# Optimization experiments

Measured on AMD Instinct MI355X. Metric: run time of the kernel, lower is better.

## Reference

```python
import jax, jax.numpy as jnp
import numpy as np

L, N1, N2 = 2, 2, 2
E1 = sum(1 + i for i in range(N1))      # 3 first-stage DAG edges per layer
E2 = sum(N1 + i for i in range(N2))     # 5 last-stage DAG edges per layer
DIM, IN_DIM, NUM_CLASSES = 256, 128, 10
N_NODES, N_EDGES, N_GRAPHS = 8000, 128000, 64


def setup_inputs():
    key = jax.random.key(0)
    ks = jax.random.split(key, 16)
    s = 0.05  # weight scale to keep activations bounded through stacked cells
    return {
        'h': jax.random.normal(ks[0], (N_NODES, IN_DIM), jnp.float32),
        'W_emb': jax.random.normal(ks[1], (IN_DIM, DIM), jnp.float32) * s,
        'b_emb': jnp.zeros((DIM,), jnp.float32),
        'Wf_dense': jax.random.normal(ks[2], (L, E1, DIM, DIM), jnp.float32) * s,
        'bf_dense': jnp.zeros((L, E1, DIM), jnp.float32),
        'Wf_sparse': jax.random.normal(ks[3], (L, E1, DIM, DIM), jnp.float32) * s,
        'bf_sparse': jnp.zeros((L, E1, DIM), jnp.float32),
        'Wl_dense': jax.random.normal(ks[4], (L, E2, DIM, DIM), jnp.float32) * s,
        'bl_dense': jnp.zeros((L, E2, DIM), jnp.float32),
        'Wl_sparse': jax.random.normal(ks[5], (L, E2, DIM, DIM), jnp.float32) * s,
        'bl_sparse': jnp.zeros((L, E2, DIM), jnp.float32),
        'a_first': 0.001 * jax.random.normal(ks[6], (L * E1, 4), jnp.float32),
        'a_mid': 0.001 * jax.random.normal(ks[7], (L * N1, 4), jnp.float32),
        'a_last': 0.001 * jax.random.normal(ks[8], (L * E2, 4), jnp.float32),
        'C1': jax.random.normal(ks[9], (DIM, DIM // 2), jnp.float32) * s,
        'c1b': jnp.zeros((DIM // 2,), jnp.float32),
        'C2': jax.random.normal(ks[10], (DIM // 2, DIM // 4), jnp.float32) * s,
        'c2b': jnp.zeros((DIM // 4,), jnp.float32),
        'C3': jax.random.normal(ks[11], (DIM // 4, NUM_CLASSES), jnp.float32) * s,
        'c3b': jnp.zeros((NUM_CLASSES,), jnp.float32),
        'src': jax.random.randint(ks[12], (N_EDGES,), 0, N_NODES, jnp.int32),
        'dst': jax.random.randint(ks[13], (N_EDGES,), 0, N_NODES, jnp.int32),
        'graph_ids': jnp.sort(jax.random.randint(ks[14], (N_NODES,), 0, N_GRAPHS, jnp.int32)),
        'num_graphs': N_GRAPHS,
    }


def forward(h, W_emb, b_emb, Wf_dense, bf_dense, Wf_sparse, bf_sparse,
            Wl_dense, bl_dense, Wl_sparse, bl_sparse, a_first, a_mid, a_last,
            C1, c1b, C2, c2b, C3, c3b, src, dst, graph_ids, num_graphs):
    N = h.shape[0]
    deg0 = jax.ops.segment_sum(jnp.ones((src.shape[0],), h.dtype), dst, num_segments=N)
    deg = jnp.maximum(deg0, 1.0)[:, None]      # in-degree, clamped for mean
    has_nb = (deg0 > 0)[:, None]

    # DARTS softmax over candidate ops (per DAG edge)
    wf = jax.nn.softmax(a_first, axis=1)
    wm = jax.nn.softmax(a_mid, axis=1)
    wl = jax.nn.softmax(a_last, axis=1)

    def mixed(xj, w, Wd, bd, Ws, bs):
        # mixture over {f_zero, f_identity, f_dense, f_sparse}
        dense = xj @ Wd + bd
        agg = jax.ops.segment_sum(xj[src], dst, num_segments=N) / deg  # mean msg-passing
        sparse = agg @ Ws + bs
        return w[1] * xj + w[2] * dense + w[3] * sparse  # w[0]*zero omitted

    x = h @ W_emb + b_emb  # embedding (Linear, data_type='gc')
    for l in range(L):
        # first stage: DAG over N1 intermediate nodes
        states = [x]
        e = 0
        for n in range(1, N1 + 1):
            s = jnp.zeros_like(x)
            for j in range(n):
                s = s + mixed(states[j], wf[l * E1 + e], Wf_dense[l, e], bf_dense[l, e],
                              Wf_sparse[l, e], bf_sparse[l, e])
                e += 1
            states.append(jax.nn.relu(s))
        # middle stage: mixture over {identity, max, mean, sum} neighbor aggregators
        mids = []
        for n in range(N1):
            xn = states[n + 1]
            w = wm[l * N1 + n]
            msg = xn[src]
            msum = jax.ops.segment_sum(msg, dst, num_segments=N)
            mmean = msum / deg
            mmax = jnp.where(has_nb, jax.ops.segment_max(msg, dst, num_segments=N), 0.0)
            mids.append(w[0] * xn + w[1] * mmax + w[2] * mmean + w[3] * msum)
        # last stage: DAG over N2 output nodes, inputs = middle states + prior lasts
        lasts = []
        e = 0
        for n in range(N2):
            ins = mids + lasts
            s = jnp.zeros_like(x)
            for j in range(N1 + n):
                s = s + mixed(ins[j], wl[l * E2 + e], Wl_dense[l, e], bl_dense[l, e],
                              Wl_sparse[l, e], bl_sparse[l, e])
                e += 1
            lasts.append(jax.nn.relu(s))
        x = x + sum(lasts) / float(N2)  # residual cell output

    # dgl.mean_nodes readout: per-graph mean over nodes
    cnt = jnp.maximum(jax.ops.segment_sum(jnp.ones((N,), x.dtype), graph_ids,
                                          num_segments=num_graphs), 1.0)[:, None]
    hg = jax.ops.segment_sum(x, graph_ids, num_segments=num_graphs) / cnt
    # MLPReadout: 256 -> 128 -> 64 -> 10
    y = jax.nn.relu(hg @ C1 + c1b)
    y = jax.nn.relu(y @ C2 + c2b)
    return y @ C3 + c3b


def reference(h, W_emb, b_emb, Wf_dense, bf_dense, Wf_sparse, bf_sparse,
              Wl_dense, bl_dense, Wl_sparse, bl_sparse, a_first, a_mid, a_last,
              C1, c1b, C2, c2b, C3, c3b, src, dst, graph_ids, num_graphs):
    return forward(h, W_emb, b_emb, Wf_dense, bf_dense, Wf_sparse, bf_sparse,
                   Wl_dense, bl_dense, Wl_sparse, bl_sparse, a_first, a_mid, a_last,
                   C1, c1b, C2, c2b, C3, c3b, src, dst, graph_ids, num_graphs)
```

## Files before the change

kernel.cpp:

```cpp
#include <hip/hip_runtime.h>

#define N_NODES   8000
#define M_PAD     8192
#define PADR      (M_PAD - N_NODES)
#define N_EDGES   128000
#define N_GRAPHS  64
#define DIM       256
#define IN_DIM    128

typedef short bf16x8 __attribute__((ext_vector_type(8)));
typedef float f32x4 __attribute__((ext_vector_type(4)));

static __device__ __forceinline__ float bf2f(unsigned v) {
  return __uint_as_float(v << 16);
}
static __device__ __forceinline__ unsigned f2bf(float f) {
  unsigned u = __float_as_uint(f);
  return (u + 0x7fffu + ((u >> 16) & 1u)) >> 16;
}

__global__ __launch_bounds__(256) void k_init(int* __restrict__ counts,
                                              unsigned short* __restrict__ hpad,
                                              unsigned short* __restrict__ p0,
                                              unsigned short* __restrict__ p1,
                                              unsigned short* __restrict__ p2,
                                              unsigned short* __restrict__ p3) {
  int i = blockIdx.x * 256 + threadIdx.x;
  if (i < N_NODES) counts[i] = 0;
  if (i < PADR * IN_DIM) hpad[i] = 0;
  if (i < PADR * DIM) { p0[i] = 0; p1[i] = 0; p2[i] = 0; p3[i] = 0; }
}

__global__ __launch_bounds__(256) void k_count(const int* __restrict__ dst,
                                               int* __restrict__ counts) {
  int e = blockIdx.x * 256 + threadIdx.x;
  if (e < N_EDGES) atomicAdd(&counts[dst[e]], 1);
}

__global__ __launch_bounds__(256) void k_scan(const int* __restrict__ counts,
                                              int* __restrict__ row_ofs,
                                              int* __restrict__ cursor,
                                              float* __restrict__ invdeg) {
  __shared__ int chunk[256];
  const int per = (N_NODES + 255) / 256;
  int t = threadIdx.x;
  int base = t * per;
  int s = 0;
  for (int i = 0; i < per; ++i) {
    int idx = base + i;
    if (idx < N_NODES) s += counts[idx];
  }
  chunk[t] = s;
  __syncthreads();
  for (int off = 1; off < 256; off <<= 1) {
    int v = 0;
    if (t >= off) v = chunk[t - off];
    __syncthreads();
    if (t >= off) chunk[t] += v;
    __syncthreads();
  }
  int run = (t > 0) ? chunk[t - 1] : 0;
  for (int i = 0; i < per; ++i) {
    int idx = base + i;
    if (idx < N_NODES) {
      row_ofs[idx] = run;
      cursor[idx] = run;
      int c = counts[idx];
      invdeg[idx] = 1.0f / (float)(c > 1 ? c : 1);
      run += c;
    }
  }
  if (t == 0) row_ofs[N_NODES] = chunk[255];
}

__global__ __launch_bounds__(256) void k_fill(const int* __restrict__ src,
                                              const int* __restrict__ dst,
                                              int* __restrict__ cursor,
                                              int* __restrict__ csr_src) {
  int e = blockIdx.x * 256 + threadIdx.x;
  if (e < N_EDGES) {
    int p = atomicAdd(&cursor[dst[e]], 1);
    csr_src[p] = src[e];
  }
}

__global__ __launch_bounds__(64) void k_softmax(const float* __restrict__ af,
                                                const float* __restrict__ am,
                                                const float* __restrict__ al,
                                                float* __restrict__ w) {
  int t = threadIdx.x;
  const float* sp;
  float* dp;
  if (t < 6)       { sp = af + t * 4;        dp = w + t * 4; }
  else if (t < 10) { sp = am + (t - 6) * 4;  dp = w + 24 + (t - 6) * 4; }
  else if (t < 20) { sp = al + (t - 10) * 4; dp = w + 40 + (t - 10) * 4; }
  else return;
  float a0 = sp[0], a1 = sp[1], a2 = sp[2], a3 = sp[3];
  float m = fmaxf(fmaxf(a0, a1), fmaxf(a2, a3));
  float e0 = expf(a0 - m), e1 = expf(a1 - m), e2 = expf(a2 - m), e3 = expf(a3 - m);
  float si = 1.0f / (e0 + e1 + e2 + e3);
  dp[0] = e0 * si; dp[1] = e1 * si; dp[2] = e2 * si; dp[3] = e3 * si;
}

__global__ __launch_bounds__(256) void k_cvt_bf16(const float* __restrict__ in,
                                                  unsigned short* __restrict__ out,
                                                  int n) {
  int i = blockIdx.x * 256 + threadIdx.x;
  if (i < n) out[i] = (unsigned short)f2bf(in[i]);
}

__global__ __launch_bounds__(256) void k_transpose_cvt(const float* __restrict__ in,
                                                       unsigned short* __restrict__ out,
                                                       int K, int N) {
  __shared__ float tile[32][33];
  int k0 = blockIdx.x * 32, n0 = blockIdx.y * 32;
  int tx = threadIdx.x & 31, ty = threadIdx.x >> 5;
#pragma unroll
  for (int i = 0; i < 4; ++i)
    tile[ty + 8 * i][tx] = in[(size_t)(k0 + ty + 8 * i) * N + n0 + tx];
  __syncthreads();
#pragma unroll
  for (int i = 0; i < 4; ++i)
    out[(size_t)(n0 + ty + 8 * i) * K + k0 + tx] =
        (unsigned short)f2bf(tile[tx][ty + 8 * i]);
}

__global__ __launch_bounds__(256) void k_transpose_cvt32(const float* __restrict__ Wfd,
                                                         const float* __restrict__ Wfs,
                                                         const float* __restrict__ Wld,
                                                         const float* __restrict__ Wls,
                                                         const float* __restrict__ wsoft,
                                                         unsigned short* __restrict__ out) {
  __shared__ float tile[32][33];
  int z = blockIdx.z;
  const float* in;
  float coef;
  const float* wf = wsoft;
  const float* wl = wsoft + 40;
  if (z < 6)       { in = Wfd + (size_t)z * DIM * DIM;        coef = wf[z * 4 + 2]; }
  else if (z < 12) { in = Wfs + (size_t)(z - 6) * DIM * DIM;  coef = wf[(z - 6) * 4 + 3]; }
  else if (z < 22) { in = Wld + (size_t)(z - 12) * DIM * DIM; coef = wl[(z - 12) * 4 + 2]; }
  else             { in = Wls + (size_t)(z - 22) * DIM * DIM; coef = wl[(z - 22) * 4 + 3]; }
  unsigned short* o = out + (size_t)z * DIM * DIM;
  int k0 = blockIdx.x * 32, n0 = blockIdx.y * 32;
  int tx = threadIdx.x & 31, ty = threadIdx.x >> 5;
#pragma unroll
  for (int i = 0; i < 4; ++i)
    tile[ty + 8 * i][tx] = in[(size_t)(k0 + ty + 8 * i) * DIM + n0 + tx];
  __syncthreads();
#pragma unroll
  for (int i = 0; i < 4; ++i)
    o[(size_t)(n0 + ty + 8 * i) * DIM + k0 + tx] =
        (unsigned short)f2bf(coef * tile[tx][ty + 8 * i]);
}

#define SEG_ACC(u) \
  { s0 += bf2f((u).x & 0xffffu); s1 += bf2f((u).x >> 16); \
    s2 += bf2f((u).y & 0xffffu); s3 += bf2f((u).y >> 16); }

#define MID_ACC(u) \
  { float v0 = bf2f((u).x & 0xffffu), v1 = bf2f((u).x >> 16); \
    float v2 = bf2f((u).y & 0xffffu), v3 = bf2f((u).y >> 16); \
    s0 += v0; s1 += v1; s2 += v2; s3 += v3; \
    m0 = fmaxf(m0, v0); m1 = fmaxf(m1, v1); \
    m2 = fmaxf(m2, v2); m3 = fmaxf(m3, v3); }

__global__ __launch_bounds__(256) void k_segmean_bf(const unsigned short* __restrict__ X,
                                                    const int* __restrict__ row_ofs,
                                                    const int* __restrict__ csr_src,
                                                    const float* __restrict__ invdeg,
                                                    unsigned short* __restrict__ out) {
  int node = blockIdx.x * 4 + (threadIdx.x >> 6);
  int l = threadIdx.x & 63;
  if (node >= N_NODES) return;
  int beg = row_ofs[node], end = row_ofs[node + 1];
  float s0 = 0.f, s1 = 0.f, s2 = 0.f, s3 = 0.f;
  int e = beg;
  for (; e + 8 <= end; e += 8) {
    int i0 = csr_src[e], i1 = csr_src[e + 1], i2 = csr_src[e + 2], i3 = csr_src[e + 3];
    int i4 = csr_src[e + 4], i5 = csr_src[e + 5], i6 = csr_src[e + 6], i7 = csr_src[e + 7];
    uint2 u0 = *(const uint2*)&X[(size_t)i0 * DIM + 4 * l];
    uint2 u1 = *(const uint2*)&X[(size_t)i1 * DIM + 4 * l];
    uint2 u2 = *(const uint2*)&X[(size_t)i2 * DIM + 4 * l];
    uint2 u3 = *(const uint2*)&X[(size_t)i3 * DIM + 4 * l];
    uint2 u4 = *(const uint2*)&X[(size_t)i4 * DIM + 4 * l];
    uint2 u5 = *(const uint2*)&X[(size_t)i5 * DIM + 4 * l];
    uint2 u6 = *(const uint2*)&X[(size_t)i6 * DIM + 4 * l];
    uint2 u7 = *(const uint2*)&X[(size_t)i7 * DIM + 4 * l];
    SEG_ACC(u0) SEG_ACC(u1) SEG_ACC(u2) SEG_ACC(u3)
    SEG_ACC(u4) SEG_ACC(u5) SEG_ACC(u6) SEG_ACC(u7)
  }
  for (; e + 4 <= end; e += 4) {
    int i0 = csr_src[e], i1 = csr_src[e + 1], i2 = csr_src[e + 2], i3 = csr_src[e + 3];
    uint2 u0 = *(const uint2*)&X[(size_t)i0 * DIM + 4 * l];
    uint2 u1 = *(const uint2*)&X[(size_t)i1 * DIM + 4 * l];
    uint2 u2 = *(const uint2*)&X[(size_t)i2 * DIM + 4 * l];
    uint2 u3 = *(const uint2*)&X[(size_t)i3 * DIM + 4 * l];
    SEG_ACC(u0) SEG_ACC(u1) SEG_ACC(u2) SEG_ACC(u3)
  }
  for (; e < end; ++e) {
    uint2 u = *(const uint2*)&X[(size_t)csr_src[e] * DIM + 4 * l];
    SEG_ACC(u)
  }
  float iv = invdeg[node];
  uint2 o;
  o.x = f2bf(s0 * iv) | (f2bf(s1 * iv) << 16);
  o.y = f2bf(s2 * iv) | (f2bf(s3 * iv) << 16);
  *(uint2*)&out[(size_t)node * DIM + 4 * l] = o;
}

__global__ __launch_bounds__(256) void k_segmean2_bf(const unsigned short* __restrict__ X0,
                                                     const unsigned short* __restrict__ X1,
                                                     const int* __restrict__ row_ofs,
                                                     const int* __restrict__ csr_src,
                                                     const float* __restrict__ invdeg,
                                                     unsigned short* __restrict__ out0,
                                                     unsigned short* __restrict__ out1) {
  int node = blockIdx.x * 4 + (threadIdx.x >> 6);
  int l = threadIdx.x & 63;
  if (node >= N_NODES) return;
  int beg = row_ofs[node], end = row_ofs[node + 1];
  float a0 = 0.f, a1 = 0.f, a2 = 0.f, a3 = 0.f;
  float b0 = 0.f, b1 = 0.f, b2 = 0.f, b3 = 0.f;
  int e = beg;
  for (; e + 4 <= end; e += 4) {
    size_t r0 = (size_t)csr_src[e] * DIM + 4 * l;
    size_t r1 = (size_t)csr_src[e + 1] * DIM + 4 * l;
    size_t r2 = (size_t)csr_src[e + 2] * DIM + 4 * l;
    size_t r3 = (size_t)csr_src[e + 3] * DIM + 4 * l;
    uint2 u0 = *(const uint2*)&X0[r0];
    uint2 u1 = *(const uint2*)&X0[r1];
    uint2 u2 = *(const uint2*)&X0[r2];
    uint2 u3 = *(const uint2*)&X0[r3];
    uint2 v0 = *(const uint2*)&X1[r0];
    uint2 v1 = *(const uint2*)&X1[r1];
    uint2 v2 = *(const uint2*)&X1[r2];
    uint2 v3 = *(const uint2*)&X1[r3];
    a0 += bf2f(u0.x & 0xffffu) + bf2f(u1.x & 0xffffu) + bf2f(u2.x & 0xffffu) + bf2f(u3.x & 0xffffu);
    a1 += bf2f(u0.x >> 16) + bf2f(u1.x >> 16) + bf2f(u2.x >> 16) + bf2f(u3.x >> 16);
    a2 += bf2f(u0.y & 0xffffu) + bf2f(u1.y & 0xffffu) + bf2f(u2.y & 0xffffu) + bf2f(u3.y & 0xffffu);
    a3 += bf2f(u0.y >> 16) + bf2f(u1.y >> 16) + bf2f(u2.y >> 16) + bf2f(u3.y >> 16);
    b0 += bf2f(v0.x & 0xffffu) + bf2f(v1.x & 0xffffu) + bf2f(v2.x & 0xffffu) + bf2f(v3.x & 0xffffu);
    b1 += bf2f(v0.x >> 16) + bf2f(v1.x >> 16) + bf2f(v2.x >> 16) + bf2f(v3.x >> 16);
    b2 += bf2f(v0.y & 0xffffu) + bf2f(v1.y & 0xffffu) + bf2f(v2.y & 0xffffu) + bf2f(v3.y & 0xffffu);
    b3 += bf2f(v0.y >> 16) + bf2f(v1.y >> 16) + bf2f(v2.y >> 16) + bf2f(v3.y >> 16);
  }
  for (; e < end; ++e) {
    size_t rb = (size_t)csr_src[e] * DIM + 4 * l;
    uint2 u = *(const uint2*)&X0[rb];
    uint2 v = *(const uint2*)&X1[rb];
    a0 += bf2f(u.x & 0xffffu); a1 += bf2f(u.x >> 16);
    a2 += bf2f(u.y & 0xffffu); a3 += bf2f(u.y >> 16);
    b0 += bf2f(v.x & 0xffffu); b1 += bf2f(v.x >> 16);
    b2 += bf2f(v.y & 0xffffu); b3 += bf2f(v.y >> 16);
  }
  float iv = invdeg[node];
  uint2 o;
  o.x = f2bf(a0 * iv) | (f2bf(a1 * iv) << 16);
  o.y = f2bf(a2 * iv) | (f2bf(a3 * iv) << 16);
  *(uint2*)&out0[(size_t)node * DIM + 4 * l] = o;
  o.x = f2bf(b0 * iv) | (f2bf(b1 * iv) << 16);
  o.y = f2bf(b2 * iv) | (f2bf(b3 * iv) << 16);
  *(uint2*)&out1[(size_t)node * DIM + 4 * l] = o;
}

__global__ __launch_bounds__(256) void k_segmid_bf(const unsigned short* __restrict__ Xn,
                                                   const int* __restrict__ row_ofs,
                                                   const int* __restrict__ csr_src,
                                                   const float* __restrict__ invdeg,
                                                   const float* __restrict__ wrow,
                                                   unsigned short* __restrict__ mean_out,
                                                   unsigned short* __restrict__ mids_out) {
  int node = blockIdx.x * 4 + (threadIdx.x >> 6);
  int l = threadIdx.x & 63;
  if (node >= N_NODES) return;
  int beg = row_ofs[node], end = row_ofs[node + 1];
  float s0 = 0.f, s1 = 0.f, s2 = 0.f, s3 = 0.f;
  float m0 = 0.f, m1 = 0.f, m2 = 0.f, m3 = 0.f;
  int e = beg;
  for (; e + 8 <= end; e += 8) {
    int i0 = csr_src[e], i1 = csr_src[e + 1], i2 = csr_src[e + 2], i3 = csr_src[e + 3];
    int i4 = csr_src[e + 4], i5 = csr_src[e + 5], i6 = csr_src[e + 6], i7 = csr_src[e + 7];
    uint2 u0 = *(const uint2*)&Xn[(size_t)i0 * DIM + 4 * l];
    uint2 u1 = *(const uint2*)&Xn[(size_t)i1 * DIM + 4 * l];
    uint2 u2 = *(const uint2*)&Xn[(size_t)i2 * DIM + 4 * l];
    uint2 u3 = *(const uint2*)&Xn[(size_t)i3 * DIM + 4 * l];
    uint2 u4 = *(const uint2*)&Xn[(size_t)i4 * DIM + 4 * l];
    uint2 u5 = *(const uint2*)&Xn[(size_t)i5 * DIM + 4 * l];
    uint2 u6 = *(const uint2*)&Xn[(size_t)i6 * DIM + 4 * l];
    uint2 u7 = *(const uint2*)&Xn[(size_t)i7 * DIM + 4 * l];
    MID_ACC(u0) MID_ACC(u1) MID_ACC(u2) MID_ACC(u3)
    MID_ACC(u4) MID_ACC(u5) MID_ACC(u6) MID_ACC(u7)
  }
  for (; e + 4 <= end; e += 4) {
    int i0 = csr_src[e], i1 = csr_src[e + 1], i2 = csr_src[e + 2], i3 = csr_src[e + 3];
    uint2 u0 = *(const uint2*)&Xn[(size_t)i0 * DIM + 4 * l];
    uint2 u1 = *(const uint2*)&Xn[(size_t)i1 * DIM + 4 * l];
    uint2 u2 = *(const uint2*)&Xn[(size_t)i2 * DIM + 4 * l];
    uint2 u3 = *(const uint2*)&Xn[(size_t)i3 * DIM + 4 * l];
    MID_ACC(u0) MID_ACC(u1) MID_ACC(u2) MID_ACC(u3)
  }
  for (; e < end; ++e) {
    uint2 u = *(const uint2*)&Xn[(size_t)csr_src[e] * DIM + 4 * l];
    MID_ACC(u)
  }
  float iv = invdeg[node];
  float e0 = s0 * iv, e1 = s1 * iv, e2 = s2 * iv, e3 = s3 * iv;
  if (mean_out) {
    uint2 o;
    o.x = f2bf(e0) | (f2bf(e1) << 16);
    o.y = f2bf(e2) | (f2bf(e3) << 16);
    *(uint2*)&mean_out[(size_t)node * DIM + 4 * l] = o;
  }
  float w0 = wrow[0], w1 = wrow[1], w2 = wrow[2], w3 = wrow[3];
  uint2 xu = *(const uint2*)&Xn[(size_t)node * DIM + 4 * l];
  float x0 = bf2f(xu.x & 0xffffu), x1 = bf2f(xu.x >> 16);
  float x2 = bf2f(xu.y & 0xffffu), x3 = bf2f(xu.y >> 16);
  uint2 o;
  o.x = f2bf(w0 * x0 + w1 * m0 + w2 * e0 + w3 * s0) |
        (f2bf(w0 * x1 + w1 * m1 + w2 * e1 + w3 * s1) << 16);
  o.y = f2bf(w0 * x2 + w1 * m2 + w2 * e2 + w3 * s2) |
        (f2bf(w0 * x3 + w1 * m3 + w2 * e3 + w3 * s3) << 16);
  *(uint2*)&mids_out[(size_t)node * DIM + 4 * l] = o;
}

struct GemmDescW {
  const unsigned short* A[4];
  const unsigned short* W[2][4];
  const float* b[2][4];
  const float* c[2][4];
  const unsigned short* I[2];
  const float* ic[2][2];
  const float* pre[2];
  const float* resid[2];
  const unsigned short* addl[2];
  float* out_f32[2];
  unsigned short* out_bf[2];
  int nmat, nid, K, relu[2], colshift;
};

__global__ __launch_bounds__(256) void k_gemm_mfma(GemmDescW d) {
  __shared__ __align__(16) unsigned short As[2][64][72];
  __shared__ __align__(16) unsigned short Bs[2][64][72];
  const int tid = threadIdx.x;
  const int b = blockIdx.x;
  const int cs = d.colshift;
  const int c = (b >> 3) & ((1 << cs) - 1);
  const int bm = ((b & 7) + 8 * (b >> (3 + cs))) * 64;
  const int half = c >> 2;
  const int bn = (c & 3) * 64;
  const int w = tid >> 6, l = tid & 63;
  const int wm = (w >> 1) * 32, wn = (w & 1) * 32;
  const int lr = l & 15, lk = (l >> 4) * 8;
  const int ldr = tid >> 3, ldk = (tid & 7) * 8;

  const int K = d.K;
  const int kds = (K == 256) ? 2 : 1;
  const int kmask = (1 << kds) - 1;
  const int nsteps = d.nmat << kds;

  f32x4 zero = {0.f, 0.f, 0.f, 0.f};
  f32x4 acc[2][2];
  acc[0][0] = zero; acc[0][1] = zero; acc[1][0] = zero; acc[1][1] = zero;

  auto gload = [&](int s, uint4& a0, uint4& a1, uint4& b0, uint4& b1) {
    int t = s >> kds;
    int k0 = (s & kmask) << 6;
    const unsigned short* __restrict__ A = d.A[t];
    const unsigned short* __restrict__ W = d.W[half][t];
    a0 = *(const uint4*)&A[(size_t)(bm + ldr) * K + k0 + ldk];
    a1 = *(const uint4*)&A[(size_t)(bm + ldr + 32) * K + k0 + ldk];
    b0 = *(const uint4*)&W[(size_t)(bn + ldr) * K + k0 + ldk];
    b1 = *(const uint4*)&W[(size_t)(bn + ldr + 32) * K + k0 + ldk];
  };

  {
    uint4 a0, a1, b0, b1;
    gload(0, a0, a1, b0, b1);
    *(uint4*)&As[0][ldr][ldk] = a0;
    *(uint4*)&As[0][ldr + 32][ldk] = a1;
    *(uint4*)&Bs[0][ldr][ldk] = b0;
    *(uint4*)&Bs[0][ldr + 32][ldk] = b1;
  }
  __syncthreads();

  int buf = 0;
  for (int s = 0; s < nsteps; ++s) {
    uint4 na0, na1, nb0, nb1;
    const bool more = (s + 1 < nsteps);
    if (more) gload(s + 1, na0, na1, nb0, nb1);
#pragma unroll
    for (int ks = 0; ks < 2; ++ks) {
      bf16x8 a0 = *(const bf16x8*)&As[buf][wm + lr][ks * 32 + lk];
      bf16x8 a1 = *(const bf16x8*)&As[buf][wm + 16 + lr][ks * 32 + lk];
      bf16x8 b0 = *(const bf16x8*)&Bs[buf][wn + lr][ks * 32 + lk];
      bf16x8 b1 = *(const bf16x8*)&Bs[buf][wn + 16 + lr][ks * 32 + lk];
      acc[0][0] = __builtin_amdgcn_mfma_f32_16x16x32_bf16(a0, b0, acc[0][0], 0, 0, 0);
      acc[0][1] = __builtin_amdgcn_mfma_f32_16x16x32_bf16(a0, b1, acc[0][1], 0, 0, 0);
      acc[1][0] = __builtin_amdgcn_mfma_f32_16x16x32_bf16(a1, b0, acc[1][0], 0, 0, 0);
      acc[1][1] = __builtin_amdgcn_mfma_f32_16x16x32_bf16(a1, b1, acc[1][1], 0, 0, 0);
    }
    if (more) {
      *(uint4*)&As[buf ^ 1][ldr][ldk] = na0;
      *(uint4*)&As[buf ^ 1][ldr + 32][ldk] = na1;
      *(uint4*)&Bs[buf ^ 1][ldr][ldk] = nb0;
      *(uint4*)&Bs[buf ^ 1][ldr + 32][ldk] = nb1;
    }
    __syncthreads();
    buf ^= 1;
  }

  float bias[2] = {0.f, 0.f};
  for (int t = 0; t < d.nmat; ++t) {
    const float* bp = d.b[half][t];
    if (bp) {
      float cc = d.c[half][t] ? *d.c[half][t] : 1.0f;
      bias[0] += cc * bp[bn + wn + lr];
      bias[1] += cc * bp[bn + wn + 16 + lr];
    }
  }
  float vout[2][2][4];
#pragma unroll
  for (int m = 0; m < 2; ++m)
#pragma unroll
    for (int n = 0; n < 2; ++n)
#pragma unroll
      for (int i = 0; i < 4; ++i) vout[m][n][i] = acc[m][n][i] + bias[n];
#pragma unroll
  for (int u = 0; u < 2; ++u) {
    if (u < d.nid) {
      float icu = *d.ic[half][u];
      const unsigned short* __restrict__ I = d.I[u];
#pragma unroll
      for (int m = 0; m < 2; ++m)
#pragma unroll
        for (int n = 0; n < 2; ++n)
#pragma unroll
          for (int i = 0; i < 4; ++i) {
            int row = bm + wm + m * 16 + (l >> 4) * 4 + i;
            int col = bn + wn + n * 16 + lr;
            vout[m][n][i] += icu * bf2f(I[(size_t)row * DIM + col]);
          }
    }
  }
  const float* pre = d.pre[half];
  const float* resid = d.resid[half];
  const unsigned short* addl = d.addl[half];
  unsigned short* obf = d.out_bf[half];
  float* of32 = d.out_f32[half];
  const int do_relu = d.relu[half];
#pragma unroll
  for (int m = 0; m < 2; ++m)
#pragma unroll
    for (int n = 0; n < 2; ++n)
#pragma unroll
      for (int i = 0; i < 4; ++i) {
        int row = bm + wm + m * 16 + (l >> 4) * 4 + i;
        int col = bn + wn + n * 16 + lr;
        size_t idx = (size_t)row * DIM + col;
        float v = vout[m][n][i];
        if (pre) v += pre[idx];
        if (do_relu) v = fmaxf(v, 0.f);
        if (resid) v = resid[idx] + 0.5f * (bf2f(addl[idx]) + v);
        if (obf) obf[idx] = (unsigned short)f2bf(v);
        if (of32) of32[idx] = v;
      }
}

__global__ __launch_bounds__(256) void k_readout_mlp(const float* __restrict__ x,
                                                     const int* __restrict__ gid,
                                                     const float* __restrict__ C1,
                                                     const float* __restrict__ c1b,
                                                     const float* __restrict__ C2,
                                                     const float* __restrict__ c2b,
                                                     const float* __restrict__ C3,
                                                     const float* __restrict__ c3b,
                                                     float* __restrict__ out) {
  int g = blockIdx.x, t = threadIdx.x;
  int lo = 0, hi = N_NODES;
  while (lo < hi) { int m = (lo + hi) >> 1; if (gid[m] < g) lo = m + 1; else hi = m; }
  int beg = lo;
  lo = beg; hi = N_NODES;
  while (lo < hi) { int m = (lo + hi) >> 1; if (gid[m] <= g) lo = m + 1; else hi = m; }
  int end = lo;
  float s0 = 0.f, s1 = 0.f, s2 = 0.f, s3 = 0.f;
  float s4 = 0.f, s5 = 0.f, s6 = 0.f, s7 = 0.f;
  int i = beg;
  for (; i + 8 <= end; i += 8) {
    s0 += x[(size_t)(i + 0) * DIM + t];
    s1 += x[(size_t)(i + 1) * DIM + t];
    s2 += x[(size_t)(i + 2) * DIM + t];
    s3 += x[(size_t)(i + 3) * DIM + t];
    s4 += x[(size_t)(i + 4) * DIM + t];
    s5 += x[(size_t)(i + 5) * DIM + t];
    s6 += x[(size_t)(i + 6) * DIM + t];
    s7 += x[(size_t)(i + 7) * DIM + t];
  }
  for (; i < end; ++i) s0 += x[(size_t)i * DIM + t];
  float s = ((s0 + s1) + (s2 + s3)) + ((s4 + s5) + (s6 + s7));
  int cnt = end - beg;
  __shared__ float h0[256], h1[128], h2[64];
  h0[t] = s / (float)(cnt > 1 ? cnt : 1);
  __syncthreads();
  if (t < 128) {
    float v = c1b[t];
    for (int k = 0; k < 256; ++k) v = fmaf(h0[k], C1[k * 128 + t], v);
    h1[t] = fmaxf(v, 0.f);
  }
  __syncthreads();
  if (t < 64) {
    float v = c2b[t];
    for (int k = 0; k < 128; ++k) v = fmaf(h1[k], C2[k * 64 + t], v);
    h2[t] = fmaxf(v, 0.f);
  }
  __syncthreads();
  if (t < 10) {
    float v = c3b[t];
    for (int k = 0; k < 64; ++k) v = fmaf(h2[k], C3[k * 10 + t], v);
    out[g * 10 + t] = v;
  }
}

extern "C" void kernel_launch(void* const* d_in, const int* in_sizes, int n_in,
                              void* d_out, int out_size, void* d_ws, size_t ws_size,
                              hipStream_t stream) {
  const float* h     = (const float*)d_in[0];
  const float* W_emb = (const float*)d_in[1];
  const float* b_emb = (const float*)d_in[2];
  const float* Wf_d  = (const float*)d_in[3];
  const float* bf_d  = (const float*)d_in[4];
  const float* Wf_s  = (const float*)d_in[5];
  const float* bf_s  = (const float*)d_in[6];
  const float* Wl_d  = (const float*)d_in[7];
  const float* bl_d  = (const float*)d_in[8];
  const float* Wl_s  = (const float*)d_in[9];
  const float* bl_s  = (const float*)d_in[10];
  const float* a_first = (const float*)d_in[11];
  const float* a_mid   = (const float*)d_in[12];
  const float* a_last  = (const float*)d_in[13];
  const float* C1 = (const float*)d_in[14];
  const float* c1b = (const float*)d_in[15];
  const float* C2 = (const float*)d_in[16];
  const float* c2b = (const float*)d_in[17];
  const float* C3 = (const float*)d_in[18];
  const float* c3b = (const float*)d_in[19];
  const int* src = (const int*)d_in[20];
  const int* dst = (const int*)d_in[21];
  const int* gid = (const int*)d_in[22];
  (void)in_sizes; (void)n_in; (void)out_size; (void)ws_size;

  char* p = (char*)d_ws;
  auto alloc = [&](size_t bytes) {
    void* r = (void*)p;
    p += (bytes + 255) & ~(size_t)255;
    return r;
  };
  typedef unsigned short u16;
  const size_t NBF = (size_t)M_PAD * DIM * sizeof(u16);
  float* x_f32  = (float*)alloc((size_t)M_PAD * DIM * sizeof(float));
  float* s2part = (float*)alloc((size_t)M_PAD * DIM * sizeof(float));
  float* xpart  = (float*)alloc((size_t)M_PAD * DIM * sizeof(float));
  u16* xb    = (u16*)alloc(NBF);
  u16* s1b   = (u16*)alloc(NBF);
  u16* s2b   = (u16*)alloc(NBF);
  u16* m0b   = (u16*)alloc(NBF);
  u16* m1b   = (u16*)alloc(NBF);
  u16* l0b   = (u16*)alloc(NBF);
  u16* aggAb = (u16*)alloc(NBF);
  u16* aggBb = (u16*)alloc(NBF);
  u16* h_bf  = (u16*)alloc((size_t)M_PAD * IN_DIM * sizeof(u16));
  u16* WT    = (u16*)alloc((size_t)(DIM * IN_DIM + 32 * DIM * DIM) * sizeof(u16));
  u16* WTe   = WT;
  u16* WTfd  = WT + DIM * IN_DIM;
  u16* WTfs  = WTfd + 6 * DIM * DIM;
  u16* WTld  = WTfs + 6 * DIM * DIM;
  u16* WTls  = WTld + 10 * DIM * DIM;
  float* invdeg = (float*)alloc(N_NODES * sizeof(float));
  int* counts  = (int*)alloc(N_NODES * sizeof(int));
  int* row_ofs = (int*)alloc((N_NODES + 1) * sizeof(int));
  int* cursor  = (int*)alloc(N_NODES * sizeof(int));
  int* csr_src = (int*)alloc(N_EDGES * sizeof(int));
  float* wsoft = (float*)alloc(80 * sizeof(float));

  const int EB = (N_EDGES + 255) / 256;

  k_init<<<192, 256, 0, stream>>>(
      counts, h_bf + (size_t)N_NODES * IN_DIM,
      aggAb + (size_t)N_NODES * DIM, aggBb + (size_t)N_NODES * DIM,
      m0b + (size_t)N_NODES * DIM, m1b + (size_t)N_NODES * DIM);

  k_count<<<EB, 256, 0, stream>>>(dst, counts);
  k_scan<<<1, 256, 0, stream>>>(counts, row_ofs, cursor, invdeg);
  k_fill<<<EB, 256, 0, stream>>>(src, dst, cursor, csr_src);
  k_softmax<<<1, 64, 0, stream>>>(a_first, a_mid, a_last, wsoft);

  const float* wf = wsoft;
  const float* wm = wsoft + 24;
  const float* wl = wsoft + 40;

  k_cvt_bf16<<<(N_NODES * IN_DIM + 255) / 256, 256, 0, stream>>>(h, h_bf, N_NODES * IN_DIM);
  k_transpose_cvt<<<dim3(IN_DIM / 32, DIM / 32, 1), 256, 0, stream>>>(W_emb, WTe, IN_DIM, DIM);
  k_transpose_cvt32<<<dim3(8, 8, 32), 256, 0, stream>>>(Wf_d, Wf_s, Wl_d, Wl_s, wsoft, WTfd);

  const int GG1 = (M_PAD / 64) * 4;
  const int GG2 = (M_PAD / 64) * 8;
  const int SB = (N_NODES + 3) / 4;

  {
    GemmDescW d{};
    d.A[0] = h_bf; d.W[0][0] = WTe; d.b[0][0] = b_emb;
    d.nmat = 1; d.nid = 0; d.K = IN_DIM; d.colshift = 2;
    d.out_f32[0] = x_f32; d.out_bf[0] = xb;
    k_gemm_mfma<<<GG1, 256, 0, stream>>>(d);
  }

  for (int l = 0; l < 2; ++l) {
    auto WFD = [&](int e) { return WTfd + (size_t)(l * 3 + e) * DIM * DIM; };
    auto BFD = [&](int e) { return bf_d + (size_t)(l * 3 + e) * DIM; };
    auto WFS = [&](int e) { return WTfs + (size_t)(l * 3 + e) * DIM * DIM; };
    auto BFS = [&](int e) { return bf_s + (size_t)(l * 3 + e) * DIM; };
    auto WLD = [&](int e) { return WTld + (size_t)(l * 5 + e) * DIM * DIM; };
    auto BLD = [&](int e) { return bl_d + (size_t)(l * 5 + e) * DIM; };
    auto WLS = [&](int e) { return WTls + (size_t)(l * 5 + e) * DIM * DIM; };
    auto BLS = [&](int e) { return bl_s + (size_t)(l * 5 + e) * DIM; };
    auto WFrow = [&](int e) { return wf + (l * 3 + e) * 4; };
    auto WMrow = [&](int n) { return wm + (l * 2 + n) * 4; };
    auto WLrow = [&](int e) { return wl + (l * 5 + e) * 4; };

    k_segmean_bf<<<SB, 256, 0, stream>>>(xb, row_ofs, csr_src, invdeg, aggAb);

    {
      GemmDescW d{};
      d.A[0] = xb; d.A[1] = aggAb; d.nmat = 2; d.K = DIM; d.colshift = 3;
      d.I[0] = xb; d.nid = 1;
      d.W[0][0] = WFD(0); d.b[0][0] = BFD(0); d.c[0][0] = WFrow(0) + 2;
      d.W[0][1] = WFS(0); d.b[0][1] = BFS(0); d.c[0][1] = WFrow(0) + 3;
      d.ic[0][0] = WFrow(0) + 1; d.relu[0] = 1; d.out_bf[0] = s1b;
      d.W[1][0] = WFD(1); d.b[1][0] = BFD(1); d.c[1][0] = WFrow(1) + 2;
      d.W[1][1] = WFS(1); d.b[1][1] = BFS(1); d.c[1][1] = WFrow(1) + 3;
      d.ic[1][0] = WFrow(1) + 1; d.relu[1] = 0; d.out_f32[1] = s2part;
      k_gemm_mfma<<<GG2, 256, 0, stream>>>(d);
    }

    k_segmid_bf<<<SB, 256, 0, stream>>>(s1b, row_ofs, csr_src, invdeg, WMrow(0), aggBb, m0b);

    {
      GemmDescW d{};
      d.A[0] = s1b; d.A[1] = aggBb; d.nmat = 2; d.K = DIM; d.colshift = 2;
      d.I[0] = s1b; d.nid = 1;
      d.W[0][0] = WFD(2); d.b[0][0] = BFD(2); d.c[0][0] = WFrow(2) + 2;
      d.W[0][1] = WFS(2); d.b[0][1] = BFS(2); d.c[0][1] = WFrow(2) + 3;
      d.ic[0][0] = WFrow(2) + 1; d.pre[0] = s2part; d.relu[0] = 1; d.out_bf[0] = s2b;
      k_gemm_mfma<<<GG1, 256, 0, stream>>>(d);
    }

    k_segmid_bf<<<SB, 256, 0, stream>>>(s2b, row_ofs, csr_src, invdeg, WMrow(1), nullptr, m1b);

    k_segmean2_bf<<<SB, 256, 0, stream>>>(m0b, m1b, row_ofs, csr_src, invdeg, aggAb, aggBb);

    {
      GemmDescW d{};
      d.A[0] = m0b; d.A[1] = aggAb; d.A[2] = m1b; d.A[3] = aggBb;
      d.nmat = 4; d.K = DIM; d.colshift = 3;
      d.I[0] = m0b; d.I[1] = m1b; d.nid = 2;
      d.W[0][0] = WLD(0); d.b[0][0] = BLD(0); d.c[0][0] = WLrow(0) + 2;
      d.W[0][1] = WLS(0); d.b[0][1] = BLS(0); d.c[0][1] = WLrow(0) + 3;
      d.W[0][2] = WLD(1); d.b[0][2] = BLD(1); d.c[0][2] = WLrow(1) + 2;
      d.W[0][3] = WLS(1); d.b[0][3] = BLS(1); d.c[0][3] = WLrow(1) + 3;
      d.ic[0][0] = WLrow(0) + 1; d.ic[0][1] = WLrow(1) + 1;
      d.relu[0] = 1; d.out_bf[0] = l0b;
      d.W[1][0] = WLD(2); d.b[1][0] = BLD(2); d.c[1][0] = WLrow(2) + 2;
      d.W[1][1] = WLS(2); d.b[1][1] = BLS(2); d.c[1][1] = WLrow(2) + 3;
      d.W[1][2] = WLD(3); d.b[1][2] = BLD(3); d.c[1][2] = WLrow(3) + 2;
      d.W[1][3] = WLS(3); d.b[1][3] = BLS(3); d.c[1][3] = WLrow(3) + 3;
      d.ic[1][0] = WLrow(2) + 1; d.ic[1][1] = WLrow(3) + 1;
      d.relu[1] = 0; d.out_f32[1] = xpart;
      k_gemm_mfma<<<GG2, 256, 0, stream>>>(d);
    }

    k_segmean_bf<<<SB, 256, 0, stream>>>(l0b, row_ofs, csr_src, invdeg, s1b);

    {
      GemmDescW d{};
      d.A[0] = l0b; d.A[1] = s1b; d.nmat = 2; d.K = DIM; d.colshift = 2;
      d.I[0] = l0b; d.nid = 1;
      d.W[0][0] = WLD(4); d.b[0][0] = BLD(4); d.c[0][0] = WLrow(4) + 2;
      d.W[0][1] = WLS(4); d.b[0][1] = BLS(4); d.c[0][1] = WLrow(4) + 3;
      d.ic[0][0] = WLrow(4) + 1; d.pre[0] = xpart; d.relu[0] = 1;
      d.resid[0] = x_f32; d.addl[0] = l0b;
      d.out_f32[0] = x_f32; d.out_bf[0] = xb;
      k_gemm_mfma<<<GG1, 256, 0, stream>>>(d);
    }
  }

  k_readout_mlp<<<N_GRAPHS, 256, 0, stream>>>(x_f32, gid, C1, c1b, C2, c2b, C3, c3b,
                                              (float*)d_out);
}
```

Measured before the change: 326.9 us.

## Prefetch two k-steps ahead in MFMA GEMM and merge embedding weight transpose launch

The GEMM main loop is restructured into a two-step unrolled pipeline that keeps two register stages of global loads in flight, so global memory latency is hidden further ahead of the MFMA work. nsteps is always even (nmat<<kds with kds>=1), so the paired loop covers every step. The separate W_emb transpose kernel is folded into the batched weight transpose kernel as an extra z-slice, removing one launch. The deeper prefetch raises register pressure, which could lower occupancy.

```diff
diff --git a/kernel.cpp b/kernel.cpp
--- a/kernel.cpp
+++ b/kernel.cpp
@@ -109,30 +109,30 @@
   if (i < n) out[i] = (unsigned short)f2bf(in[i]);
 }
 
-__global__ __launch_bounds__(256) void k_transpose_cvt(const float* __restrict__ in,
-                                                       unsigned short* __restrict__ out,
-                                                       int K, int N) {
-  __shared__ float tile[32][33];
-  int k0 = blockIdx.x * 32, n0 = blockIdx.y * 32;
-  int tx = threadIdx.x & 31, ty = threadIdx.x >> 5;
-#pragma unroll
-  for (int i = 0; i < 4; ++i)
-    tile[ty + 8 * i][tx] = in[(size_t)(k0 + ty + 8 * i) * N + n0 + tx];
-  __syncthreads();
-#pragma unroll
-  for (int i = 0; i < 4; ++i)
-    out[(size_t)(n0 + ty + 8 * i) * K + k0 + tx] =
-        (unsigned short)f2bf(tile[tx][ty + 8 * i]);
-}
-
-__global__ __launch_bounds__(256) void k_transpose_cvt32(const float* __restrict__ Wfd,
+__global__ __launch_bounds__(256) void k_transpose_cvt33(const float* __restrict__ Wfd,
                                                          const float* __restrict__ Wfs,
                                                          const float* __restrict__ Wld,
                                                          const float* __restrict__ Wls,
                                                          const float* __restrict__ wsoft,
-                                                         unsigned short* __restrict__ out) {
+                                                         unsigned short* __restrict__ out,
+                                                         const float* __restrict__ W_emb,
+                                                         unsigned short* __restrict__ WTe) {
   __shared__ float tile[32][33];
   int z = blockIdx.z;
+  int tx = threadIdx.x & 31, ty = threadIdx.x >> 5;
+  if (z == 32) {
+    if (blockIdx.x >= 4) return;
+    int k0 = blockIdx.x * 32, n0 = blockIdx.y * 32;
+#pragma unroll
+    for (int i = 0; i < 4; ++i)
+      tile[ty + 8 * i][tx] = W_emb[(size_t)(k0 + ty + 8 * i) * DIM + n0 + tx];
+    __syncthreads();
+#pragma unroll
+    for (int i = 0; i < 4; ++i)
+      WTe[(size_t)(n0 + ty + 8 * i) * IN_DIM + k0 + tx] =
+          (unsigned short)f2bf(tile[tx][ty + 8 * i]);
+    return;
+  }
   const float* in;
   float coef;
   const float* wf = wsoft;
@@ -143,7 +143,6 @@
   else             { in = Wls + (size_t)(z - 22) * DIM * DIM; coef = wl[(z - 22) * 4 + 3]; }
   unsigned short* o = out + (size_t)z * DIM * DIM;
   int k0 = blockIdx.x * 32, n0 = blockIdx.y * 32;
-  int tx = threadIdx.x & 31, ty = threadIdx.x >> 5;
 #pragma unroll
   for (int i = 0; i < 4; ++i)
     tile[ty + 8 * i][tx] = in[(size_t)(k0 + ty + 8 * i) * DIM + n0 + tx];
@@ -373,42 +372,47 @@
     b0 = *(const uint4*)&W[(size_t)(bn + ldr) * K + k0 + ldk];
     b1 = *(const uint4*)&W[(size_t)(bn + ldr + 32) * K + k0 + ldk];
   };
-
-  {
-    uint4 a0, a1, b0, b1;
-    gload(0, a0, a1, b0, b1);
-    *(uint4*)&As[0][ldr][ldk] = a0;
-    *(uint4*)&As[0][ldr + 32][ldk] = a1;
-    *(uint4*)&Bs[0][ldr][ldk] = b0;
-    *(uint4*)&Bs[0][ldr + 32][ldk] = b1;
-  }
+  auto lstore = [&](int buf, uint4 a0, uint4 a1, uint4 b0, uint4 b1) {
+    *(uint4*)&As[buf][ldr][ldk] = a0;
+    *(uint4*)&As[buf][ldr + 32][ldk] = a1;
+    *(uint4*)&Bs[buf][ldr][ldk] = b0;
+    *(uint4*)&Bs[buf][ldr + 32][ldk] = b1;
+  };
+
+  uint4 ra0, ra1, ra2, ra3;
+  uint4 rb0, rb1, rb2, rb3;
+
+  gload(0, ra0, ra1, ra2, ra3);
+  gload(1, rb0, rb1, rb2, rb3);
+  lstore(0, ra0, ra1, ra2, ra3);
   __syncthreads();
 
-  int buf = 0;
-  for (int s = 0; s < nsteps; ++s) {
-    uint4 na0, na1, nb0, nb1;
-    const bool more = (s + 1 < nsteps);
-    if (more) gload(s + 1, na0, na1, nb0, nb1);
-#pragma unroll
-    for (int ks = 0; ks < 2; ++ks) {
-      bf16x8 a0 = *(const bf16x8*)&As[buf][wm + lr][ks * 32 + lk];
-      bf16x8 a1 = *(const bf16x8*)&As[buf][wm + 16 + lr][ks * 32 + lk];
-      bf16x8 b0 = *(const bf16x8*)&Bs[buf][wn + lr][ks * 32 + lk];
-      bf16x8 b1 = *(const bf16x8*)&Bs[buf][wn + 16 + lr][ks * 32 + lk];
-      acc[0][0] = __builtin_amdgcn_mfma_f32_16x16x32_bf16(a0, b0, acc[0][0], 0, 0, 0);
-      acc[0][1] = __builtin_amdgcn_mfma_f32_16x16x32_bf16(a0, b1, acc[0][1], 0, 0, 0);
-      acc[1][0] = __builtin_amdgcn_mfma_f32_16x16x32_bf16(a1, b0, acc[1][0], 0, 0, 0);
-      acc[1][1] = __builtin_amdgcn_mfma_f32_16x16x32_bf16(a1, b1, acc[1][1], 0, 0, 0);
-    }
-    if (more) {
-      *(uint4*)&As[buf ^ 1][ldr][ldk] = na0;
-      *(uint4*)&As[buf ^ 1][ldr + 32][ldk] = na1;
-      *(uint4*)&Bs[buf ^ 1][ldr][ldk] = nb0;
-      *(uint4*)&Bs[buf ^ 1][ldr + 32][ldk] = nb1;
-    }
+#define MFMA_STEP(BUF)                                                            \
+  {                                                                               \
+    _Pragma("unroll")                                                             \
+    for (int ks = 0; ks < 2; ++ks) {                                              \
+      bf16x8 a0 = *(const bf16x8*)&As[BUF][wm + lr][ks * 32 + lk];                \
+      bf16x8 a1 = *(const bf16x8*)&As[BUF][wm + 16 + lr][ks * 32 + lk];           \
+      bf16x8 b0 = *(const bf16x8*)&Bs[BUF][wn + lr][ks * 32 + lk];                \
+      bf16x8 b1 = *(const bf16x8*)&Bs[BUF][wn + 16 + lr][ks * 32 + lk];           \
+      acc[0][0] = __builtin_amdgcn_mfma_f32_16x16x32_bf16(a0, b0, acc[0][0], 0, 0, 0); \
+      acc[0][1] = __builtin_amdgcn_mfma_f32_16x16x32_bf16(a0, b1, acc[0][1], 0, 0, 0); \
+      acc[1][0] = __builtin_amdgcn_mfma_f32_16x16x32_bf16(a1, b0, acc[1][0], 0, 0, 0); \
+      acc[1][1] = __builtin_amdgcn_mfma_f32_16x16x32_bf16(a1, b1, acc[1][1], 0, 0, 0); \
+    }                                                                             \
+  }
+
+  for (int s = 0; s < nsteps; s += 2) {
+    if (s + 2 < nsteps) gload(s + 2, ra0, ra1, ra2, ra3);
+    MFMA_STEP(0);
+    lstore(1, rb0, rb1, rb2, rb3);
     __syncthreads();
-    buf ^= 1;
-  }
+    if (s + 3 < nsteps) gload(s + 3, rb0, rb1, rb2, rb3);
+    MFMA_STEP(1);
+    if (s + 2 < nsteps) lstore(0, ra0, ra1, ra2, ra3);
+    __syncthreads();
+  }
+#undef MFMA_STEP
 
   float bias[2] = {0.f, 0.f};
   for (int t = 0; t < d.nmat; ++t) {
@@ -599,8 +603,8 @@
   const float* wl = wsoft + 40;
 
   k_cvt_bf16<<<(N_NODES * IN_DIM + 255) / 256, 256, 0, stream>>>(h, h_bf, N_NODES * IN_DIM);
-  k_transpose_cvt<<<dim3(IN_DIM / 32, DIM / 32, 1), 256, 0, stream>>>(W_emb, WTe, IN_DIM, DIM);
-  k_transpose_cvt32<<<dim3(8, 8, 32), 256, 0, stream>>>(Wf_d, Wf_s, Wl_d, Wl_s, wsoft, WTfd);
+  k_transpose_cvt33<<<dim3(8, 8, 33), 256, 0, stream>>>(Wf_d, Wf_s, Wl_d, Wl_s, wsoft,
+                                                        WTfd, W_emb, WTe);
 
   const int GG1 = (M_PAD / 64) * 4;
   const int GG2 = (M_PAD / 64) * 8;
```

New measurement: 324.9 us (median of 2 runs). No clear change (-0.6%).
